# Kernel tuning notes

Hardware: AMD Instinct MI355X
Metric: run time of the kernel (lower is better)

Reference implementation:

```python
import jax, jax.numpy as jnp
import numpy as np

B, SQ, SK = 2, 2048, 4096
D_STATE, D_LISTEN, D_PROJ, H = 512, 512, 512, 8


def setup_inputs() -> dict:
    key = jax.random.key(0)
    ks = jax.random.split(key, 9)
    s = 0.02
    return {
        "q": jax.random.normal(ks[0], (B, SQ, D_STATE), jnp.float32),
        "k": jax.random.normal(ks[1], (B, SK, D_LISTEN), jnp.float32),
        "mask": jax.random.randint(ks[2], (B, SK), 0, 2, jnp.int32),
        "Wq": jax.random.normal(ks[3], (D_STATE, D_PROJ), jnp.float32) * s,
        "bq": jnp.zeros((D_PROJ,), jnp.float32),
        "Wk": jax.random.normal(ks[4], (D_LISTEN, D_PROJ), jnp.float32) * s,
        "bk": jnp.zeros((D_PROJ,), jnp.float32),
        "Wv": jax.random.normal(ks[5], (D_LISTEN, D_PROJ), jnp.float32) * s,
        "bv": jnp.zeros((D_PROJ,), jnp.float32),
    }


def reference(q, k, mask, Wq, bq, Wk, bk, Wv, bv):
    # projections
    qp = q @ Wq + bq                      # [B, SQ, D]
    kp = k @ Wk + bk                      # [B, SK, D]
    vp = k @ Wv + bv                      # [B, SK, D]
    W = D_PROJ // H                        # head width
    qh = qp.reshape(B, SQ, H, W).transpose(0, 2, 1, 3)  # [B,H,SQ,W]
    kh = kp.reshape(B, SK, H, W).transpose(0, 2, 1, 3)  # [B,H,SK,W]
    vh = vp.reshape(B, SK, H, W).transpose(0, 2, 1, 3)  # [B,H,SK,W]
    scores = jnp.einsum("bhqw,bhkw->bhqk", qh, kh) / np.sqrt(W).astype(np.float32)
    m = mask[:, None, None, :].astype(jnp.float32)       # [B,1,1,SK]
    scores = scores - 10000.0 * (1.0 - m)
    attn = jax.nn.softmax(scores, axis=-1)               # dropout=0 (eval)
    h = jnp.einsum("bhqk,bhkw->bhqw", attn, vh)          # [B,H,SQ,W]
    h = h.transpose(0, 2, 1, 3).reshape(B, SQ, D_PROJ)
    return h
```

## Files before the change

kernel.cpp:

```cpp
#include <hip/hip_runtime.h>
#include <hip/hip_bf16.h>


typedef short  s16x8 __attribute__((ext_vector_type(8)));
typedef short  s16x4 __attribute__((ext_vector_type(4)));
typedef float  f32x4 __attribute__((ext_vector_type(4)));
typedef float  f32x16 __attribute__((ext_vector_type(16)));
typedef unsigned int u32;
typedef unsigned int u32x4 __attribute__((ext_vector_type(4)));

__device__ __forceinline__ unsigned short f2bf(float x) {
    return __builtin_bit_cast(unsigned short, __float2bfloat16(x));
}
__device__ __forceinline__ void gload16(const void* g, void* lds) {
    __builtin_amdgcn_global_load_lds(
        (const __attribute__((address_space(1))) unsigned int*)g,
        (__attribute__((address_space(3))) unsigned int*)lds, 16, 0, 0);
}
__device__ __forceinline__ u32 cvtpk(float lo, float hi) {
    u32 r;
    asm("v_cvt_pk_bf16_f32 %0, %1, %2" : "=v"(r) : "v"(lo), "v"(hi));
    return r;
}

__global__ __launch_bounds__(256) void prep(
    const float* __restrict__ q, const float* __restrict__ k,
    const float* __restrict__ Wq, const float* __restrict__ Wk,
    const float* __restrict__ Wv, const int* __restrict__ mask,
    unsigned short* __restrict__ qbf, unsigned short* __restrict__ kbf,
    unsigned short* __restrict__ wtq, unsigned short* __restrict__ wtk,
    unsigned short* __restrict__ wtv, int* __restrict__ cntb)
{
    __shared__ float T[64][65];
    const int bid = blockIdx.x;
    const int tid = threadIdx.x;
    if (bid < 3072) {
        const float* src = bid < 1024 ? q : k;
        unsigned short* dst = bid < 1024 ? qbf : kbf;
        int i = (bid < 1024 ? bid : bid - 1024) * 256 + tid;
        float4 a = reinterpret_cast<const float4*>(src)[2 * i];
        float4 b = reinterpret_cast<const float4*>(src)[2 * i + 1];
        s16x8 o;
        o[0] = (short)f2bf(a.x); o[1] = (short)f2bf(a.y);
        o[2] = (short)f2bf(a.z); o[3] = (short)f2bf(a.w);
        o[4] = (short)f2bf(b.x); o[5] = (short)f2bf(b.y);
        o[6] = (short)f2bf(b.z); o[7] = (short)f2bf(b.w);
        reinterpret_cast<s16x8*>(dst)[i] = o;
    } else if (bid < 3264) {
        int t = bid - 3072;
        int z = t >> 6;
        int tt = t & 63;
        const float* W = z == 0 ? Wq : z == 1 ? Wk : Wv;
        unsigned short* D = z == 0 ? wtq : z == 1 ? wtk : wtv;
        const int k0 = (tt >> 3) * 64, n0 = (tt & 7) * 64;
        const int r = tid >> 2, cq = tid & 3;
        #pragma unroll
        for (int p = 0; p < 4; ++p) {
            int c = (cq + 4 * p) * 4;
            float4 v = *reinterpret_cast<const float4*>(
                &W[(size_t)(k0 + r) * 512 + n0 + c]);
            T[c + 0][r] = v.x; T[c + 1][r] = v.y;
            T[c + 2][r] = v.z; T[c + 3][r] = v.w;
        }
        __syncthreads();
        #pragma unroll
        for (int p = 0; p < 4; ++p) {
            int kc = (cq + 4 * p) * 4;
            s16x4 o;
            o[0] = (short)f2bf(T[r][kc + 0]);
            o[1] = (short)f2bf(T[r][kc + 1]);
            o[2] = (short)f2bf(T[r][kc + 2]);
            o[3] = (short)f2bf(T[r][kc + 3]);
            *reinterpret_cast<s16x4*>(&D[(size_t)(n0 + r) * 512 + k0 + kc]) = o;
        }
    } else {
        __shared__ int red[4];
        int b = bid - 3264;
        int base = b * 4096 + tid * 16;
        int s = 0;
        #pragma unroll
        for (int p = 0; p < 4; ++p) {
            int4 m = *reinterpret_cast<const int4*>(&mask[base + 4 * p]);
            s += m.x + m.y + m.z + m.w;
        }
        #pragma unroll
        for (int off = 1; off < 64; off <<= 1)
            s += __shfl_xor(s, off);
        if ((tid & 63) == 0) red[tid >> 6] = s;
        __syncthreads();
        if (tid == 0)
            cntb[b] = 4096 - (red[0] + red[1] + red[2] + red[3]);
    }
}

__global__ __launch_bounds__(256) void proj3(
    const unsigned short* __restrict__ qbf, const unsigned short* __restrict__ kbf,
    const unsigned short* __restrict__ wtq, const unsigned short* __restrict__ wtk,
    const unsigned short* __restrict__ wtv,
    const float* __restrict__ bq, const float* __restrict__ bk,
    const float* __restrict__ bv, const int* __restrict__ mask,
    unsigned short* __restrict__ qh, unsigned short* __restrict__ kh,
    unsigned short* __restrict__ vt)
{
    __shared__ unsigned short As[2][128 * 64];
    __shared__ unsigned short Bs[2][64 * 64];

    const int tid  = threadIdx.x;
    const int wv   = tid >> 6;
    const int lane = tid & 63;
    const int g    = lane >> 4;
    const int ln   = lane & 15;
    const int swz  = (ln & 7) << 3;

    const int id = blockIdx.x;
    const unsigned short *A, *Wt;
    const float* bias;
    unsigned short* dst;
    int S, trans, nb, mb, mflag;
    if (id < 256)      { A = qbf; Wt = wtq; bias = bq; dst = qh; S = 2048; trans = 0; mflag = 0; nb = id & 7;         mb = id >> 3; }
    else if (id < 768) { A = kbf; Wt = wtk; bias = bk; dst = kh; S = 4096; trans = 0; mflag = 1; nb = (id - 256) & 7; mb = (id - 256) >> 3; }
    else               { A = kbf; Wt = wtv; bias = bv; dst = vt; S = 4096; trans = 1; mflag = 2; nb = (id - 768) & 7; mb = (id - 768) >> 3; }
    const int m0 = mb * 128, n0 = nb * 64;
    const float scl = (mflag == 0) ? 0.18033688011112042f : 1.f;

    f32x4 acc[4][2];
    #pragma unroll
    for (int i = 0; i < 4; ++i)
        #pragma unroll
        for (int j = 0; j < 2; ++j) acc[i][j] = (f32x4)0.f;

    auto stage = [&](int bufn, int k0) {
        #pragma unroll
        for (int p = 0; p < 4; ++p) {
            int slot = p * 256 + tid;
            int row = slot >> 3, cb = slot & 7;
            int cbp = cb ^ (row & 7);
            gload16(&A[(size_t)(m0 + row) * 512 + k0 + cbp * 8], &As[bufn][slot * 8]);
        }
        #pragma unroll
        for (int p = 0; p < 2; ++p) {
            int slot = p * 256 + tid;
            int row = slot >> 3, cb = slot & 7;
            int cbp = cb ^ (row & 7);
            gload16(&Wt[(size_t)(n0 + row) * 512 + k0 + cbp * 8], &Bs[bufn][slot * 8]);
        }
    };

    stage(0, 0);
    __syncthreads();
    int buf = 0;
    for (int kk = 0; kk < 8; ++kk) {
        if (kk < 7) stage(buf ^ 1, (kk + 1) * 64);
        #pragma unroll
        for (int ks = 0; ks < 2; ++ks) {
            s16x8 fa[2], fb[4];
            #pragma unroll
            for (int mi = 0; mi < 2; ++mi)
                fa[mi] = *reinterpret_cast<const s16x8*>(
                    &As[buf][((wv * 32 + 16 * mi + ln) * 64 + ks * 32 + g * 8) ^ swz]);
            #pragma unroll
            for (int nj = 0; nj < 4; ++nj)
                fb[nj] = *reinterpret_cast<const s16x8*>(
                    &Bs[buf][((16 * nj + ln) * 64 + ks * 32 + g * 8) ^ swz]);
            if (!trans) {
                #pragma unroll
                for (int mi = 0; mi < 2; ++mi)
                    #pragma unroll
                    for (int nj = 0; nj < 4; ++nj)
                        acc[nj][mi] = __builtin_amdgcn_mfma_f32_16x16x32_bf16(
                            fa[mi], fb[nj], acc[nj][mi], 0, 0, 0);
            } else {
                #pragma unroll
                for (int nj = 0; nj < 4; ++nj)
                    #pragma unroll
                    for (int mi = 0; mi < 2; ++mi)
                        acc[nj][mi] = __builtin_amdgcn_mfma_f32_16x16x32_bf16(
                            fb[nj], fa[mi], acc[nj][mi], 0, 0, 0);
            }
        }
        __syncthreads();
        buf ^= 1;
    }

    const int h    = nb;
    const int bidx = m0 / S;
    const int s0   = m0 - bidx * S;

    if (!trans) {
        float bvv[4];
        #pragma unroll
        for (int nj = 0; nj < 4; ++nj) bvv[nj] = bias[n0 + 16 * nj + ln];
        unsigned short* base = dst + (size_t)(bidx * 8 + h) * S * 64;
        #pragma unroll
        for (int mi = 0; mi < 2; ++mi)
            #pragma unroll
            for (int r = 0; r < 4; ++r) {
                int s = s0 + wv * 32 + 16 * mi + 4 * g + r;
                float fm = (mflag == 1) ? (float)mask[bidx * 4096 + s] : 1.f;
                float fs = fm * scl;
                #pragma unroll
                for (int nj = 0; nj < 4; ++nj)
                    base[(size_t)s * 64 + 16 * nj + ln] =
                        f2bf((acc[nj][mi][r] + bvv[nj]) * fs);
            }
    } else {
        float fmc[2];
        #pragma unroll
        for (int mi = 0; mi < 2; ++mi)
            fmc[mi] = (float)mask[bidx * 4096 + s0 + wv * 32 + 16 * mi + ln];
        unsigned short* base = dst + (size_t)(bidx * 8 + h) * 64 * (size_t)S;
        #pragma unroll
        for (int nj = 0; nj < 4; ++nj)
            #pragma unroll
            for (int r = 0; r < 4; ++r) {
                int w = 16 * nj + 4 * g + r;
                float bw = bias[n0 + w];
                #pragma unroll
                for (int mi = 0; mi < 2; ++mi)
                    base[(size_t)w * S + s0 + wv * 32 + 16 * mi + ln] =
                        f2bf((acc[nj][mi][r] + bw) * fmc[mi]);
            }
    }
}

__global__ __launch_bounds__(512, 1) void attn12(
    const unsigned short* __restrict__ qh,
    const unsigned short* __restrict__ kh,
    const unsigned short* __restrict__ vt,
    const int* __restrict__ cntb,
    float* __restrict__ out)
{
    __shared__ float Ored[2][4][32][36];
    __shared__ float lw[2][2][4][32];

    const int tid  = threadIdx.x;
    const int wid  = tid >> 6;
    const int kq   = wid & 3;
    const int qg   = wid >> 2;
    const int lane = tid & 63;
    const int l31  = lane & 31;
    const int h32  = lane >> 5;

    const int id  = blockIdx.x;
    const int xcd = id & 7;
    const int j   = id >> 3;
    const int bh  = xcd * 2 + (j >> 4);
    const int qt  = j & 15;
    const int b   = bh >> 3;
    const int hh  = bh & 7;

    const unsigned short* Kp = kh + (size_t)bh * 4096 * 64
                               + (size_t)(kq * 32 + l31) * 64 + h32 * 8;
    const unsigned short* Vp0 = vt + (size_t)bh * 64 * 4096
                               + (size_t)l31 * 4096 + kq * 32 + h32 * 8;

    s16x8 Qf[2][4];
    {
        const unsigned short* Qb = qh + ((size_t)bh * 2048 + qt * 128 + qg * 64) * 64;
        #pragma unroll
        for (int qt2 = 0; qt2 < 2; ++qt2)
            #pragma unroll
            for (int ks = 0; ks < 4; ++ks)
                Qf[qt2][ks] = *reinterpret_cast<const s16x8*>(
                    &Qb[(size_t)(qt2 * 32 + l31) * 64 + ks * 16 + h32 * 8]);
    }

    f32x16 O[2][2];
    #pragma unroll
    for (int i = 0; i < 2; ++i)
        #pragma unroll
        for (int jj = 0; jj < 2; ++jj) O[i][jj] = (f32x16)0.f;
    float l_acc0 = 0.f, l_acc1 = 0.f;

    s16x8 kf[4], vf[4];

    auto loadK = [&](int t) {
        #pragma unroll
        for (int ks = 0; ks < 4; ++ks)
            kf[ks] = *reinterpret_cast<const s16x8*>(Kp + (size_t)t * 8192 + ks * 16);
    };
    auto loadV = [&](int t) {
        #pragma unroll
        for (int wt = 0; wt < 2; ++wt)
            #pragma unroll
            for (int t2 = 0; t2 < 2; ++t2)
                vf[wt * 2 + t2] = *reinterpret_cast<const s16x8*>(
                    Vp0 + (size_t)wt * 32 * 4096 + t * 128 + t2 * 16);
    };
    auto QK = [&](f32x16* Sv) {
        Sv[0] = (f32x16)0.f; Sv[1] = (f32x16)0.f;
        __builtin_amdgcn_s_setprio(1);
        #pragma unroll
        for (int ks = 0; ks < 4; ++ks) {
            Sv[0] = __builtin_amdgcn_mfma_f32_32x32x16_bf16(kf[ks], Qf[0][ks], Sv[0], 0, 0, 0);
            Sv[1] = __builtin_amdgcn_mfma_f32_32x32x16_bf16(kf[ks], Qf[1][ks], Sv[1], 0, 0, 0);
        }
        __builtin_amdgcn_s_setprio(0);
    };
    auto SM = [&](const f32x16* Sv, s16x8 pa[2][2]) {
        #pragma unroll
        for (int qt2 = 0; qt2 < 2; ++qt2) {
            float pp[16];
            #pragma unroll
            for (int r = 0; r < 16; ++r)
                pp[r] = exp2f(Sv[qt2][r]);
            float ls = (((pp[0] + pp[1]) + (pp[2] + pp[3]))
                     + ((pp[4] + pp[5]) + (pp[6] + pp[7])))
                     + (((pp[8] + pp[9]) + (pp[10] + pp[11]))
                     + ((pp[12] + pp[13]) + (pp[14] + pp[15])));
            if (qt2 == 0) l_acc0 += ls; else l_acc1 += ls;
            u32 W[8];
            #pragma unroll
            for (int c = 0; c < 4; ++c) {
                W[2 * c + 0] = cvtpk(pp[4 * c + 0], pp[4 * c + 1]);
                W[2 * c + 1] = cvtpk(pp[4 * c + 2], pp[4 * c + 3]);
            }
            asm("v_permlane32_swap_b32 %0, %1" : "+v"(W[0]), "+v"(W[2]));
            asm("v_permlane32_swap_b32 %0, %1" : "+v"(W[1]), "+v"(W[3]));
            asm("v_permlane32_swap_b32 %0, %1" : "+v"(W[4]), "+v"(W[6]));
            asm("v_permlane32_swap_b32 %0, %1" : "+v"(W[5]), "+v"(W[7]));
            u32x4 lo, hi;
            lo[0] = W[0]; lo[1] = W[1]; lo[2] = W[2]; lo[3] = W[3];
            hi[0] = W[4]; hi[1] = W[5]; hi[2] = W[6]; hi[3] = W[7];
            pa[qt2][0] = __builtin_bit_cast(s16x8, lo);
            pa[qt2][1] = __builtin_bit_cast(s16x8, hi);
        }
    };
    auto PV = [&](s16x8 pa[2][2]) {
        __builtin_amdgcn_s_setprio(1);
        #pragma unroll
        for (int qt2 = 0; qt2 < 2; ++qt2)
            #pragma unroll
            for (int wt = 0; wt < 2; ++wt)
                #pragma unroll
                for (int t2 = 0; t2 < 2; ++t2)
                    O[qt2][wt] = __builtin_amdgcn_mfma_f32_32x32x16_bf16(
                        pa[qt2][t2], vf[wt * 2 + t2], O[qt2][wt], 0, 0, 0);
        __builtin_amdgcn_s_setprio(0);
    };

    f32x16 SA[2], SB[2];
    s16x8 paA[2][2], paB[2][2];

    loadK(0);
    QK(SA);
    loadK(1);
    loadV(0);

    for (int tt = 0; tt < 16; ++tt) {
        const int t0 = 2 * tt;
        QK(SB);
        if (t0 + 2 < 32) loadK(t0 + 2);
        SM(SA, paA);
        PV(paA);
        loadV(t0 + 1);
        if (t0 + 2 < 32) QK(SA);
        if (t0 + 3 < 32) loadK(t0 + 3);
        SM(SB, paB);
        PV(paB);
        if (t0 + 2 < 32) loadV(t0 + 2);
    }

    float ls0 = l_acc0 + __shfl_xor(l_acc0, 32);
    float ls1 = l_acc1 + __shfl_xor(l_acc1, 32);
    if (lane < 32) {
        lw[qg][0][kq][l31] = ls0;
        lw[qg][1][kq][l31] = ls1;
    }

    const float cnt = (float)cntb[b];
    const int grp = tid >> 8;
    const int tt  = tid & 255;
    const int qr  = tt >> 3;
    const int w8  = (tt & 7) * 4;
    #pragma unroll
    for (int qt2 = 0; qt2 < 2; ++qt2)
        #pragma unroll
        for (int wt = 0; wt < 2; ++wt) {
            __syncthreads();
            f32x16 oo = O[qt2][wt];
            #pragma unroll
            for (int r = 0; r < 16; ++r)
                Ored[qg][kq][(r & 3) + 8 * (r >> 2) + 4 * h32][l31] = oo[r];
            __syncthreads();
            float4 s  = *reinterpret_cast<const float4*>(&Ored[grp][0][qr][w8]);
            float4 s1 = *reinterpret_cast<const float4*>(&Ored[grp][1][qr][w8]);
            float4 s2 = *reinterpret_cast<const float4*>(&Ored[grp][2][qr][w8]);
            float4 s3 = *reinterpret_cast<const float4*>(&Ored[grp][3][qr][w8]);
            float l = (lw[grp][qt2][0][qr] + lw[grp][qt2][1][qr]
                     + lw[grp][qt2][2][qr] + lw[grp][qt2][3][qr]) - cnt;
            float inv = 1.f / l;
            int qglob = qt * 128 + grp * 64 + qt2 * 32 + qr;
            float4 o;
            o.x = (s.x + s1.x + s2.x + s3.x) * inv;
            o.y = (s.y + s1.y + s2.y + s3.y) * inv;
            o.z = (s.z + s1.z + s2.z + s3.z) * inv;
            o.w = (s.w + s1.w + s2.w + s3.w) * inv;
            *reinterpret_cast<float4*>(
                &out[((size_t)b * 2048 + qglob) * 512 + hh * 64 + wt * 32 + w8]) = o;
        }
}

extern "C" void kernel_launch(void* const* d_in, const int* in_sizes, int n_in,
                              void* d_out, int out_size, void* d_ws, size_t ws_size,
                              hipStream_t stream)
{
    const float* q    = (const float*)d_in[0];
    const float* k    = (const float*)d_in[1];
    const int*   mask = (const int*)  d_in[2];
    const float* Wq   = (const float*)d_in[3];
    const float* bq   = (const float*)d_in[4];
    const float* Wk   = (const float*)d_in[5];
    const float* bk   = (const float*)d_in[6];
    const float* Wv   = (const float*)d_in[7];
    const float* bv   = (const float*)d_in[8];
    float* out = (float*)d_out;

    unsigned short* p = (unsigned short*)d_ws;
    unsigned short* qh  = p; p += (size_t)2 * 8 * 2048 * 64;
    unsigned short* kh  = p; p += (size_t)2 * 8 * 4096 * 64;
    unsigned short* vt  = p; p += (size_t)2 * 8 * 4096 * 64;
    unsigned short* qbf = p; p += (size_t)2 * 2048 * 512;
    unsigned short* kbf = p; p += (size_t)2 * 4096 * 512;
    unsigned short* wtq = p; p += 512 * 512;
    unsigned short* wtk = p; p += 512 * 512;
    unsigned short* wtv = p; p += 512 * 512;
    int* cntb = (int*)p;

    dim3 blk(256);
    prep<<<dim3(3266), blk, 0, stream>>>(q, k, Wq, Wk, Wv, mask,
                                         qbf, kbf, wtq, wtk, wtv, cntb);
    proj3<<<dim3(1280), blk, 0, stream>>>(qbf, kbf, wtq, wtk, wtv,
                                          bq, bk, bv, mask, qh, kh, vt);
    attn12<<<dim3(256), dim3(512), 0, stream>>>(qh, kh, vt, cntb, out);
}
```

Baseline: 115.4 us.

## Restructure attention loop to share one score buffer and shift softmax pipeline

Replaces the two score accumulators (SA/SB) with a single shared S buffer and reorders the main loop so each softmax runs immediately after its QK and is consumed by PV one step later. This cuts live accumulator registers. It also drops the min-blocks hint from launch_bounds, which may allow more waves per SIMD. The trade-off is a tighter dependency chain between QK MFMAs and the exp/convert stage, which may reduce overlap of matrix and vector work.

```diff
diff --git a/kernel.cpp b/kernel.cpp
--- a/kernel.cpp
+++ b/kernel.cpp
@@ -223,7 +223,7 @@
     }
 }
 
-__global__ __launch_bounds__(512, 1) void attn12(
+__global__ __launch_bounds__(512) void attn13(
     const unsigned short* __restrict__ qh,
     const unsigned short* __restrict__ kh,
     const unsigned short* __restrict__ vt,
@@ -287,23 +287,27 @@
                 vf[wt * 2 + t2] = *reinterpret_cast<const s16x8*>(
                     Vp0 + (size_t)wt * 32 * 4096 + t * 128 + t2 * 16);
     };
-    auto QK = [&](f32x16* Sv) {
-        Sv[0] = (f32x16)0.f; Sv[1] = (f32x16)0.f;
+
+    f32x16 S[2];
+    s16x8 paA[2][2], paB[2][2];
+
+    auto QK = [&]() {
+        S[0] = (f32x16)0.f; S[1] = (f32x16)0.f;
         __builtin_amdgcn_s_setprio(1);
         #pragma unroll
         for (int ks = 0; ks < 4; ++ks) {
-            Sv[0] = __builtin_amdgcn_mfma_f32_32x32x16_bf16(kf[ks], Qf[0][ks], Sv[0], 0, 0, 0);
-            Sv[1] = __builtin_amdgcn_mfma_f32_32x32x16_bf16(kf[ks], Qf[1][ks], Sv[1], 0, 0, 0);
+            S[0] = __builtin_amdgcn_mfma_f32_32x32x16_bf16(kf[ks], Qf[0][ks], S[0], 0, 0, 0);
+            S[1] = __builtin_amdgcn_mfma_f32_32x32x16_bf16(kf[ks], Qf[1][ks], S[1], 0, 0, 0);
         }
         __builtin_amdgcn_s_setprio(0);
     };
-    auto SM = [&](const f32x16* Sv, s16x8 pa[2][2]) {
+    auto SM = [&](s16x8 pa[2][2]) {
         #pragma unroll
         for (int qt2 = 0; qt2 < 2; ++qt2) {
             float pp[16];
             #pragma unroll
             for (int r = 0; r < 16; ++r)
-                pp[r] = exp2f(Sv[qt2][r]);
+                pp[r] = exp2f(S[qt2][r]);
             float ls = (((pp[0] + pp[1]) + (pp[2] + pp[3]))
                      + ((pp[4] + pp[5]) + (pp[6] + pp[7])))
                      + (((pp[8] + pp[9]) + (pp[10] + pp[11]))
@@ -339,26 +343,26 @@
         __builtin_amdgcn_s_setprio(0);
     };
 
-    f32x16 SA[2], SB[2];
-    s16x8 paA[2][2], paB[2][2];
-
     loadK(0);
-    QK(SA);
+    loadV(0);
+    QK();
     loadK(1);
-    loadV(0);
+    SM(paA);
 
     for (int tt = 0; tt < 16; ++tt) {
         const int t0 = 2 * tt;
-        QK(SB);
+        QK();
         if (t0 + 2 < 32) loadK(t0 + 2);
-        SM(SA, paA);
         PV(paA);
         loadV(t0 + 1);
-        if (t0 + 2 < 32) QK(SA);
+        SM(paB);
+        if (t0 + 2 < 32) QK();
         if (t0 + 3 < 32) loadK(t0 + 3);
-        SM(SB, paB);
         PV(paB);
-        if (t0 + 2 < 32) loadV(t0 + 2);
+        if (t0 + 2 < 32) {
+            loadV(t0 + 2);
+            SM(paA);
+        }
     }
 
     float ls0 = l_acc0 + __shfl_xor(l_acc0, 32);
@@ -432,5 +436,5 @@
                                          qbf, kbf, wtq, wtk, wtv, cntb);
     proj3<<<dim3(1280), blk, 0, stream>>>(qbf, kbf, wtq, wtk, wtv,
                                           bq, bk, bv, mask, qh, kh, vt);
-    attn12<<<dim3(256), dim3(512), 0, stream>>>(qh, kh, vt, cntb, out);
-}
+    attn13<<<dim3(256), dim3(512), 0, stream>>>(qh, kh, vt, cntb, out);
+}
```

After: 106.3 us. -8.0%, faster.
